# Kernel optimization log

Measured on AMD Instinct MI355X. Metric: run time of the kernel, lower is better.

Reference implementation:

```python
import jax, jax.numpy as jnp
import numpy as np

NUM_LAYERS = 2
ALPHA = 0.5
AGGREGATION = 'mean'

def setup_inputs() -> dict:
    key = jax.random.key(0)
    k1, k2, k3, k4 = jax.random.split(key, 4)
    N, E, D = 10000, 160000, 384
    x = jax.random.normal(k1, (N, D), dtype=jnp.float32)
    edge_index = jax.random.randint(k2, (2, E), 0, N, dtype=jnp.int64)
    edge_attr = jax.random.normal(k3, (E, D), dtype=jnp.float32)
    question_emb = jax.random.normal(k4, (D,), dtype=jnp.float32)
    return {"x": x, "edge_index": edge_index, "edge_attr": edge_attr, "question_emb": question_emb}

def _l2norm(v, axis):
    return v / jnp.linalg.norm(v, axis=axis, keepdims=True).clip(1e-12)

def reference(x, edge_index, edge_attr, question_emb):
    num_nodes = x.shape[0]
    src, dst = edge_index[0], edge_index[1]
    # per-edge similarity between edge label embedding and question
    edge_sim = _l2norm(edge_attr, 1) @ _l2norm(question_emb, 0)  # [E]
    if AGGREGATION == 'mean':
        degree = jax.ops.segment_sum(jnp.ones_like(edge_sim), dst, num_segments=num_nodes)
        degree = jnp.clip(degree, 1.0, None)[:, None]  # [N,1]
    for _ in range(NUM_LAYERS):
        msgs = x[src] * edge_sim[:, None]                      # [E,D]
        x_new = jax.ops.segment_sum(msgs, dst, num_segments=num_nodes)  # [N,D]
        if AGGREGATION == 'mean':
            x_new = x_new / degree
        x = ALPHA * x + (1.0 - ALPHA) * x_new
    return x
```

## Files before the change

kernel.cpp:

```cpp
#include <hip/hip_runtime.h>
#include <hip/hip_bf16.h>

#define D 384
#define SLOTS 96

__global__ void qnorm_kernel(const float* __restrict__ q, float* __restrict__ qn) {
    __shared__ float red[8];
    int t = threadIdx.x;
    float v = q[t];
    float ss = v * v;
    for (int s = 32; s > 0; s >>= 1) ss += __shfl_down(ss, s);
    if ((t & 63) == 0) red[t >> 6] = ss;
    __syncthreads();
    if (t == 0) {
        float tot = 0.f;
        for (int i = 0; i < 6; i++) tot += red[i];
        red[0] = 1.0f / fmaxf(sqrtf(tot), 1e-12f);
    }
    __syncthreads();
    qn[t] = v * red[0];
}

__global__ __launch_bounds__(256) void edge_kernel(
        const float* __restrict__ ea, const float* __restrict__ qn,
        const int* __restrict__ src, const int* __restrict__ dst,
        int* __restrict__ cnt, int2* __restrict__ bucket, int E) {
    __shared__ float s_q[D];
    int t = threadIdx.x;
    for (int i = t; i < D; i += 256) s_q[i] = qn[i];
    __syncthreads();

    int wave = t >> 6, lane = t & 63;
    int e = blockIdx.x * 4 + wave;
    if (e >= E) return;

    const float4* row = (const float4*)(ea + (size_t)e * D);
    const float4* q4  = (const float4*)s_q;

    float dot = 0.f, ss = 0.f;
    float4 v = row[lane];
    float4 q = q4[lane];
    dot += v.x*q.x + v.y*q.y + v.z*q.z + v.w*q.w;
    ss  += v.x*v.x + v.y*v.y + v.z*v.z + v.w*v.w;
    if (lane < 32) {
        float4 v2 = row[lane + 64];
        float4 q2 = q4[lane + 64];
        dot += v2.x*q2.x + v2.y*q2.y + v2.z*q2.z + v2.w*q2.w;
        ss  += v2.x*v2.x + v2.y*v2.y + v2.z*v2.z + v2.w*v2.w;
    }
    for (int s = 32; s > 0; s >>= 1) {
        dot += __shfl_down(dot, s);
        ss  += __shfl_down(ss, s);
    }
    if (lane == 0) {
        float sim = dot / fmaxf(sqrtf(ss), 1e-12f);
        int n = dst[e];
        int p = atomicAdd(&cnt[n], 1);
        if (p < SLOTS)
            bucket[(size_t)n * SLOTS + p] = make_int2(src[e], __float_as_int(sim));
    }
}

__global__ __launch_bounds__(D) void aggregate_kernel(
        const float* __restrict__ xin, const int* __restrict__ cnt,
        const int2* __restrict__ bucket, float* __restrict__ xout, int N) {
    int n = blockIdx.x;
    int t = threadIdx.x;
    int deg = cnt[n];
    int m = min(deg, SLOTS);

    __shared__ int   s_src[SLOTS];
    __shared__ float s_sim[SLOTS];
    if (t < m) {
        int2 p = bucket[(size_t)n * SLOTS + t];
        s_src[t] = p.x;
        s_sim[t] = __int_as_float(p.y);
    }
    __syncthreads();

    float a0 = 0.f, a1 = 0.f, a2 = 0.f, a3 = 0.f;
    int k = 0;
    for (; k + 4 <= m; k += 4) {
        a0 += xin[(size_t)s_src[k    ] * D + t] * s_sim[k    ];
        a1 += xin[(size_t)s_src[k + 1] * D + t] * s_sim[k + 1];
        a2 += xin[(size_t)s_src[k + 2] * D + t] * s_sim[k + 2];
        a3 += xin[(size_t)s_src[k + 3] * D + t] * s_sim[k + 3];
    }
    for (; k < m; k++)
        a0 += xin[(size_t)s_src[k] * D + t] * s_sim[k];
    float acc = (a0 + a1) + (a2 + a3);

    float scale = 1.0f / fmaxf((float)deg, 1.0f);
    size_t idx = (size_t)n * D + t;
    xout[idx] = 0.5f * xin[idx] + 0.5f * acc * scale;
}

extern "C" void kernel_launch(void* const* d_in, const int* in_sizes, int n_in,
                              void* d_out, int out_size, void* d_ws, size_t ws_size,
                              hipStream_t stream) {
    const float* x   = (const float*)d_in[0];
    const int*   ei  = (const int*)d_in[1];
    const float* ea  = (const float*)d_in[2];
    const float* qe  = (const float*)d_in[3];

    const int N = in_sizes[0] / D;
    const int E = in_sizes[1] / 2;
    const int* src = ei;
    const int* dst = ei + E;

    char* w = (char*)d_ws;
    size_t off = 0;
    auto alloc = [&](size_t bytes) {
        char* p = w + off;
        off = (off + bytes + 255) & ~(size_t)255;
        return p;
    };
    float* qn     = (float*)alloc((size_t)D * 4);
    int*   cnt    = (int*)  alloc((size_t)N * 4);
    int2*  bucket = (int2*) alloc((size_t)N * SLOTS * 8);
    float* xbuf   = (float*)alloc((size_t)N * D * 4);
    (void)ws_size; (void)n_in; (void)out_size;

    hipMemsetAsync(cnt, 0, (size_t)N * 4, stream);
    qnorm_kernel<<<1, D, 0, stream>>>(qe, qn);
    edge_kernel<<<(E + 3) / 4, 256, 0, stream>>>(ea, qn, src, dst, cnt, bucket, E);
    aggregate_kernel<<<N, D, 0, stream>>>(x, cnt, bucket, xbuf, N);
    aggregate_kernel<<<N, D, 0, stream>>>(xbuf, cnt, bucket, (float*)d_out, N);
}
```

Baseline: 437.7 us.

## Fuse question norm into edge kernel, vectorize aggregation with float4 edge-split gathers

After: 430.5 us, median of 2. Within noise of the previous version (-1.6%).

```diff
diff --git a/kernel.cpp b/kernel.cpp
--- a/kernel.cpp
+++ b/kernel.cpp
@@ -2,49 +2,43 @@
 #include <hip/hip_bf16.h>
 
 #define D 384
+#define D4 96
 #define SLOTS 96
 
-__global__ void qnorm_kernel(const float* __restrict__ q, float* __restrict__ qn) {
-    __shared__ float red[8];
-    int t = threadIdx.x;
-    float v = q[t];
-    float ss = v * v;
-    for (int s = 32; s > 0; s >>= 1) ss += __shfl_down(ss, s);
-    if ((t & 63) == 0) red[t >> 6] = ss;
-    __syncthreads();
-    if (t == 0) {
-        float tot = 0.f;
-        for (int i = 0; i < 6; i++) tot += red[i];
-        red[0] = 1.0f / fmaxf(sqrtf(tot), 1e-12f);
-    }
-    __syncthreads();
-    qn[t] = v * red[0];
-}
+typedef float vfloat4 __attribute__((ext_vector_type(4)));
 
 __global__ __launch_bounds__(256) void edge_kernel(
-        const float* __restrict__ ea, const float* __restrict__ qn,
+        const float* __restrict__ ea, const float* __restrict__ q,
         const int* __restrict__ src, const int* __restrict__ dst,
         int* __restrict__ cnt, int2* __restrict__ bucket, int E) {
     __shared__ float s_q[D];
+    __shared__ float s_red[4];
+    __shared__ float s_invq;
     int t = threadIdx.x;
-    for (int i = t; i < D; i += 256) s_q[i] = qn[i];
+
+    float ssq = 0.f;
+    for (int i = t; i < D; i += 256) { float v = q[i]; s_q[i] = v; ssq += v * v; }
+    for (int s = 32; s > 0; s >>= 1) ssq += __shfl_down(ssq, s);
+    if ((t & 63) == 0) s_red[t >> 6] = ssq;
+    __syncthreads();
+    if (t == 0)
+        s_invq = 1.0f / fmaxf(sqrtf(s_red[0] + s_red[1] + s_red[2] + s_red[3]), 1e-12f);
     __syncthreads();
 
     int wave = t >> 6, lane = t & 63;
     int e = blockIdx.x * 4 + wave;
     if (e >= E) return;
 
-    const float4* row = (const float4*)(ea + (size_t)e * D);
-    const float4* q4  = (const float4*)s_q;
+    const vfloat4* row = (const vfloat4*)(ea + (size_t)e * D);
+    const vfloat4* q4  = (const vfloat4*)s_q;
 
-    float dot = 0.f, ss = 0.f;
-    float4 v = row[lane];
-    float4 q = q4[lane];
-    dot += v.x*q.x + v.y*q.y + v.z*q.z + v.w*q.w;
-    ss  += v.x*v.x + v.y*v.y + v.z*v.z + v.w*v.w;
+    vfloat4 v = __builtin_nontemporal_load(&row[lane]);
+    vfloat4 qq = q4[lane];
+    float dot = v.x*qq.x + v.y*qq.y + v.z*qq.z + v.w*qq.w;
+    float ss  = v.x*v.x + v.y*v.y + v.z*v.z + v.w*v.w;
     if (lane < 32) {
-        float4 v2 = row[lane + 64];
-        float4 q2 = q4[lane + 64];
+        vfloat4 v2 = __builtin_nontemporal_load(&row[lane + 64]);
+        vfloat4 q2 = q4[lane + 64];
         dot += v2.x*q2.x + v2.y*q2.y + v2.z*q2.z + v2.w*q2.w;
         ss  += v2.x*v2.x + v2.y*v2.y + v2.z*v2.z + v2.w*v2.w;
     }
@@ -53,7 +47,7 @@
         ss  += __shfl_down(ss, s);
     }
     if (lane == 0) {
-        float sim = dot / fmaxf(sqrtf(ss), 1e-12f);
+        float sim = dot * s_invq / fmaxf(sqrtf(ss), 1e-12f);
         int n = dst[e];
         int p = atomicAdd(&cnt[n], 1);
         if (p < SLOTS)
@@ -69,8 +63,9 @@
     int deg = cnt[n];
     int m = min(deg, SLOTS);
 
-    __shared__ int   s_src[SLOTS];
-    __shared__ float s_sim[SLOTS];
+    __shared__ int    s_src[SLOTS];
+    __shared__ float  s_sim[SLOTS];
+    __shared__ float4 s_red[4][D4];
     if (t < m) {
         int2 p = bucket[(size_t)n * SLOTS + t];
         s_src[t] = p.x;
@@ -78,21 +73,43 @@
     }
     __syncthreads();
 
-    float a0 = 0.f, a1 = 0.f, a2 = 0.f, a3 = 0.f;
-    int k = 0;
-    for (; k + 4 <= m; k += 4) {
-        a0 += xin[(size_t)s_src[k    ] * D + t] * s_sim[k    ];
-        a1 += xin[(size_t)s_src[k + 1] * D + t] * s_sim[k + 1];
-        a2 += xin[(size_t)s_src[k + 2] * D + t] * s_sim[k + 2];
-        a3 += xin[(size_t)s_src[k + 3] * D + t] * s_sim[k + 3];
+    const float4* xin4 = (const float4*)xin;
+    int g = t / D4, r = t - g * D4;
+
+    float4 a0 = make_float4(0.f, 0.f, 0.f, 0.f);
+    float4 a1 = make_float4(0.f, 0.f, 0.f, 0.f);
+    int k = g;
+    for (; k + 4 < m; k += 8) {
+        float4 v0 = xin4[(size_t)s_src[k]     * D4 + r];
+        float4 v1 = xin4[(size_t)s_src[k + 4] * D4 + r];
+        float  w0 = s_sim[k], w1 = s_sim[k + 4];
+        a0.x += v0.x*w0; a0.y += v0.y*w0; a0.z += v0.z*w0; a0.w += v0.w*w0;
+        a1.x += v1.x*w1; a1.y += v1.y*w1; a1.z += v1.z*w1; a1.w += v1.w*w1;
     }
-    for (; k < m; k++)
-        a0 += xin[(size_t)s_src[k] * D + t] * s_sim[k];
-    float acc = (a0 + a1) + (a2 + a3);
+    if (k < m) {
+        float4 v0 = xin4[(size_t)s_src[k] * D4 + r];
+        float  w0 = s_sim[k];
+        a0.x += v0.x*w0; a0.y += v0.y*w0; a0.z += v0.z*w0; a0.w += v0.w*w0;
+    }
+    a0.x += a1.x; a0.y += a1.y; a0.z += a1.z; a0.w += a1.w;
+    s_red[g][r] = a0;
+    __syncthreads();
 
-    float scale = 1.0f / fmaxf((float)deg, 1.0f);
-    size_t idx = (size_t)n * D + t;
-    xout[idx] = 0.5f * xin[idx] + 0.5f * acc * scale;
+    if (t < D4) {
+        float4 acc;
+        acc.x = s_red[0][t].x + s_red[1][t].x + s_red[2][t].x + s_red[3][t].x;
+        acc.y = s_red[0][t].y + s_red[1][t].y + s_red[2][t].y + s_red[3][t].y;
+        acc.z = s_red[0][t].z + s_red[1][t].z + s_red[2][t].z + s_red[3][t].z;
+        acc.w = s_red[0][t].w + s_red[1][t].w + s_red[2][t].w + s_red[3][t].w;
+        float scale = 0.5f / fmaxf((float)deg, 1.0f);
+        float4 xi = xin4[(size_t)n * D4 + t];
+        float4 o;
+        o.x = 0.5f*xi.x + acc.x*scale;
+        o.y = 0.5f*xi.y + acc.y*scale;
+        o.z = 0.5f*xi.z + acc.z*scale;
+        o.w = 0.5f*xi.w + acc.w*scale;
+        ((float4*)xout)[(size_t)n * D4 + t] = o;
+    }
 }
 
 extern "C" void kernel_launch(void* const* d_in, const int* in_sizes, int n_in,
@@ -115,15 +132,13 @@
         off = (off + bytes + 255) & ~(size_t)255;
         return p;
     };
-    float* qn     = (float*)alloc((size_t)D * 4);
     int*   cnt    = (int*)  alloc((size_t)N * 4);
     int2*  bucket = (int2*) alloc((size_t)N * SLOTS * 8);
     float* xbuf   = (float*)alloc((size_t)N * D * 4);
     (void)ws_size; (void)n_in; (void)out_size;
 
-    hipMemsetAsync(cnt, 0, (size_t)N * 4, stream);
-    qnorm_kernel<<<1, D, 0, stream>>>(qe, qn);
-    edge_kernel<<<(E + 3) / 4, 256, 0, stream>>>(ea, qn, src, dst, cnt, bucket, E);
+    (void)hipMemsetAsync(cnt, 0, (size_t)N * 4, stream);
+    edge_kernel<<<(E + 3) / 4, 256, 0, stream>>>(ea, qe, src, dst, cnt, bucket, E);
     aggregate_kernel<<<N, D, 0, stream>>>(x, cnt, bucket, xbuf, N);
     aggregate_kernel<<<N, D, 0, stream>>>(xbuf, cnt, bucket, (float*)d_out, N);
 }
```
